# Kernel optimization log

Measured on AMD Instinct MI355X. Metric: run time of the kernel, lower is better.

Reference implementation:

```python
import jax, jax.numpy as jnp
import numpy as np

T = 100000


def setup_inputs() -> dict:
    key = jax.random.key(0)
    u = jax.random.normal(key, (1, T, 2), dtype=jnp.float32)
    M = jnp.array([20.0, 10.0], dtype=jnp.float32)
    C = jnp.array([10.0, 10.0, 10.0], dtype=jnp.float32)   # trainable damping
    K = jnp.array([2000.0, 1000.0, 5000.0], dtype=jnp.float32)
    x0 = jnp.zeros((1, 4), dtype=jnp.float32)              # [y1, v1, y2, v2]
    dt = jnp.asarray(0.002, dtype=jnp.float32)
    return {"u": u, "M": M, "C": C, "K": K, "x0": x0, "dt": dt}


def reference(u, M, C, K, x0, dt):
    # 2x2 coupled damping / stiffness matrices (same math as _fun)
    Cm = jnp.stack([jnp.stack([C[0] + C[1], -C[1]]),
                    jnp.stack([-C[1], C[2] + C[1]])])
    Km = jnp.stack([jnp.stack([K[0] + K[1], -K[1]]),
                    jnp.stack([-K[1], K[2] + K[1]])])

    def accel(z, v, ut):  # z, v, ut: [2]
        return (ut - Cm @ v - Km @ z) / M

    def step(carry, ut):
        y, v = carry
        k1 = accel(y, v, ut)
        y2 = y + v * (dt / 2.0); v2 = v + k1 * (dt / 2.0)
        k2 = accel(y2, v2, ut)
        y3 = y + v2 * (dt / 2.0); v3 = v + k2 * (dt / 2.0)
        k3 = accel(y3, v3, ut)
        y4 = y + v3 * dt; v4 = v + k3 * dt
        k4 = accel(y4, v4, ut)
        yn = y + (dt / 6.0) * (v + 2.0 * v2 + 2.0 * v3 + v4)
        vn = v + (dt / 6.0) * (k1 + 2.0 * k2 + 2.0 * k3 + k4)
        return (yn, vn), yn

    y0 = x0[0, ::2]   # positions [y1, y2]
    v0 = x0[0, 1::2]  # velocities [v1, v2]
    _, ys = jax.lax.scan(step, (y0, v0), u[0])  # ys: [T, 2]
    return ys[None]  # [1, T, 2] position sequence, matching RNN output y
```

## Files before the change

### kernel.cpp

```cpp
#include <hip/hip_runtime.h>


#define L_LOG2   6
#define L_CHUNK  64
#define SEG      8
#define NSEG     256
#define NCHUNK   (NSEG * SEG)
#define SMAX     16
#define NLEV     (SMAX - L_LOG2 + 1)

__device__ inline void accel_d(const double* M, const double* Cm, const double* Km,
                               const double* u, const double* z, const double* v, double* a) {
  a[0] = (u[0] - Cm[0] * v[0] - Cm[1] * v[1] - Km[0] * z[0] - Km[1] * z[1]) / M[0];
  a[1] = (u[1] - Cm[2] * v[0] - Cm[3] * v[1] - Km[2] * z[0] - Km[3] * z[1]) / M[1];
}

__device__ inline void rk4_step_d(const double* M, const double* Cm, const double* Km,
                                  double dt, double* y, double* v, const double* u) {
  double k1[2], k2[2], k3[2], k4[2];
  double y2[2], v2[2], y3[2], v3[2], y4[2], v4[2];
  double h = dt * 0.5;
  accel_d(M, Cm, Km, u, y, v, k1);
  y2[0] = y[0] + v[0] * h;  y2[1] = y[1] + v[1] * h;
  v2[0] = v[0] + k1[0] * h; v2[1] = v[1] + k1[1] * h;
  accel_d(M, Cm, Km, u, y2, v2, k2);
  y3[0] = y[0] + v2[0] * h;  y3[1] = y[1] + v2[1] * h;
  v3[0] = v[0] + k2[0] * h;  v3[1] = v[1] + k2[1] * h;
  accel_d(M, Cm, Km, u, y3, v3, k3);
  y4[0] = y[0] + v3[0] * dt; y4[1] = y[1] + v3[1] * dt;
  v4[0] = v[0] + k3[0] * dt; v4[1] = v[1] + k3[1] * dt;
  accel_d(M, Cm, Km, u, y4, v4, k4);
  double s = dt / 6.0;
  double yn0 = y[0] + s * (v[0] + 2.0 * v2[0] + 2.0 * v3[0] + v4[0]);
  double yn1 = y[1] + s * (v[1] + 2.0 * v2[1] + 2.0 * v3[1] + v4[1]);
  double vn0 = v[0] + s * (k1[0] + 2.0 * k2[0] + 2.0 * k3[0] + k4[0]);
  double vn1 = v[1] + s * (k1[1] + 2.0 * k2[1] + 2.0 * k3[1] + k4[1]);
  y[0] = yn0; y[1] = yn1; v[0] = vn0; v[1] = vn1;
}

__device__ inline void build_cols(const float* Mp, const float* Cp, const float* Kp,
                                  const float* dtp, float* Af, float* Bf, double* Ad) {
  int tid = threadIdx.x;
  if (tid < 6) {
    double M[2]  = {(double)Mp[0], (double)Mp[1]};
    double Cm[4] = {(double)Cp[0] + (double)Cp[1], -(double)Cp[1],
                    -(double)Cp[1], (double)Cp[2] + (double)Cp[1]};
    double Km[4] = {(double)Kp[0] + (double)Kp[1], -(double)Kp[1],
                    -(double)Kp[1], (double)Kp[2] + (double)Kp[1]};
    double dt = (double)dtp[0];
    double y[2] = {0, 0}, v[2] = {0, 0}, u[2] = {0, 0};
    if      (tid == 0) y[0] = 1.0;
    else if (tid == 1) y[1] = 1.0;
    else if (tid == 2) v[0] = 1.0;
    else if (tid == 3) v[1] = 1.0;
    else if (tid == 4) u[0] = 1.0;
    else               u[1] = 1.0;
    rk4_step_d(M, Cm, Km, dt, y, v, u);
    if (tid < 4) {
      if (Af) {
        Af[0 * 4 + tid] = (float)y[0]; Af[1 * 4 + tid] = (float)y[1];
        Af[2 * 4 + tid] = (float)v[0]; Af[3 * 4 + tid] = (float)v[1];
      }
      if (Ad) {
        Ad[0 * 4 + tid] = y[0]; Ad[1 * 4 + tid] = y[1];
        Ad[2 * 4 + tid] = v[0]; Ad[3 * 4 + tid] = v[1];
      }
    } else if (Bf) {
      int j = tid - 4;
      Bf[0 * 2 + j] = (float)y[0]; Bf[1 * 2 + j] = (float)y[1];
      Bf[2 * 2 + j] = (float)v[0]; Bf[3 * 2 + j] = (float)v[1];
    }
  }
}

__device__ inline float4 mv4(const float* A, float4 x) {
  float4 r;
  r.x = A[0]  * x.x + A[1]  * x.y + A[2]  * x.z + A[3]  * x.w;
  r.y = A[4]  * x.x + A[5]  * x.y + A[6]  * x.z + A[7]  * x.w;
  r.z = A[8]  * x.x + A[9]  * x.y + A[10] * x.z + A[11] * x.w;
  r.w = A[12] * x.x + A[13] * x.y + A[14] * x.z + A[15] * x.w;
  return r;
}
__device__ inline float4 f4add(float4 a, float4 b) {
  return make_float4(a.x + b.x, a.y + b.y, a.z + b.z, a.w + b.w);
}
__device__ inline float4 stepf(const float* a, const float* b, float4 s, float2 ut) {
  float4 r;
  r.x = a[0]  * s.x + a[1]  * s.y + a[2]  * s.z + a[3]  * s.w + b[0] * ut.x + b[1] * ut.y;
  r.y = a[4]  * s.x + a[5]  * s.y + a[6]  * s.z + a[7]  * s.w + b[2] * ut.x + b[3] * ut.y;
  r.z = a[8]  * s.x + a[9]  * s.y + a[10] * s.z + a[11] * s.w + b[4] * ut.x + b[5] * ut.y;
  r.w = a[12] * s.x + a[13] * s.y + a[14] * s.z + a[15] * s.w + b[6] * ut.x + b[7] * ut.y;
  return r;
}

__global__ __launch_bounds__(256) void kOffsets(
    const float* __restrict__ u, const float* M, const float* C, const float* K,
    const float* dtp, int T, float4* __restrict__ c_arr) {
  __shared__ float Af[16], Bf[8];
  build_cols(M, C, K, dtp, Af, Bf, nullptr);
  __syncthreads();
  float a[16], b[8];
#pragma unroll
  for (int e = 0; e < 16; ++e) a[e] = Af[e];
#pragma unroll
  for (int e = 0; e < 8; ++e) b[e] = Bf[e];

  int j  = blockIdx.x * blockDim.x + threadIdx.x;
  int t0 = j * L_CHUNK;
  const float2* u2 = (const float2*)u;
  float4 c = make_float4(0.f, 0.f, 0.f, 0.f);
  if (t0 + L_CHUNK <= T) {
#pragma unroll 4
    for (int i = 0; i < L_CHUNK; ++i) c = stepf(a, b, c, u2[t0 + i]);
  } else {
    for (int i = 0; i < L_CHUNK; ++i) {
      int t = t0 + i;
      if (t >= T) break;
      c = stepf(a, b, c, u2[t]);
    }
  }
  c_arr[j] = c;
}

__global__ __launch_bounds__(NSEG) void kScan(
    const float* M, const float* C, const float* K, const float* dtp,
    const float* x0, int T, const float4* __restrict__ c_arr, float4* __restrict__ s_arr) {
  __shared__ double Ad[16];
  __shared__ float  Gp[NLEV][16];
  __shared__ float4 S[NSEG];
  build_cols(M, C, K, dtp, nullptr, nullptr, Ad);
  __syncthreads();

  int tid = threadIdx.x;
  if (tid < 16) {
    double m = Ad[tid];
    int i = tid >> 2, j = tid & 3;
#pragma unroll
    for (int lvl = 1; lvl <= SMAX; ++lvl) {
      double acc = 0.0;
#pragma unroll
      for (int k = 0; k < 4; ++k)
        acc += __shfl(m, i * 4 + k) * __shfl(m, k * 4 + j);
      m = acc;
      if (lvl >= L_LOG2) Gp[lvl - L_LOG2][tid] = (float)m;
    }
  }
  __syncthreads();

  float G[16];
#pragma unroll
  for (int e = 0; e < 16; ++e) G[e] = Gp[0][e];

  float4 cj[SEG];
  int sbase = tid * SEG;
#pragma unroll
  for (int r = 0; r < SEG; ++r) cj[r] = c_arr[sbase + r];
  float4 o = cj[0];
#pragma unroll
  for (int r = 1; r < SEG; ++r) o = f4add(mv4(G, o), cj[r]);

  if (tid == 0) {
    float4 s0 = make_float4(x0[0], x0[2], x0[1], x0[3]);
    o = f4add(mv4(&Gp[3][0], s0), o);
  }
  S[tid] = o;
  __syncthreads();

#pragma unroll
  for (int k = 0; k < 8; ++k) {
    int off = 1 << k;
    float4 add = make_float4(0.f, 0.f, 0.f, 0.f);
    bool act = (tid >= off);
    if (act) add = mv4(&Gp[3 + k][0], S[tid - off]);
    __syncthreads();
    if (act) S[tid] = f4add(S[tid], add);
    __syncthreads();
  }

  float4 st;
  if (tid == 0) st = make_float4(x0[0], x0[2], x0[1], x0[3]);
  else          st = S[tid - 1];
#pragma unroll
  for (int r = 0; r < SEG; ++r) {
    s_arr[sbase + r] = st;
    st = f4add(mv4(G, st), cj[r]);
  }
}

__global__ __launch_bounds__(256) void kEmit(
    const float* __restrict__ u, const float* M, const float* C, const float* K,
    const float* dtp, int T, const float4* __restrict__ s_arr, float2* __restrict__ out) {
  __shared__ float Af[16], Bf[8];
  build_cols(M, C, K, dtp, Af, Bf, nullptr);
  __syncthreads();
  float a[16], b[8];
#pragma unroll
  for (int e = 0; e < 16; ++e) a[e] = Af[e];
#pragma unroll
  for (int e = 0; e < 8; ++e) b[e] = Bf[e];

  int j  = blockIdx.x * blockDim.x + threadIdx.x;
  int t0 = j * L_CHUNK;
  const float2* u2 = (const float2*)u;
  float4 s = s_arr[j];
  if (t0 + L_CHUNK <= T) {
#pragma unroll 4
    for (int i = 0; i < L_CHUNK; ++i) {
      int t = t0 + i;
      s = stepf(a, b, s, u2[t]);
      out[t] = make_float2(s.x, s.y);
    }
  } else {
    for (int i = 0; i < L_CHUNK; ++i) {
      int t = t0 + i;
      if (t >= T) break;
      s = stepf(a, b, s, u2[t]);
      out[t] = make_float2(s.x, s.y);
    }
  }
}

__global__ void kSerialAll(const float* u, const float* Mp, const float* Cp, const float* Kp,
                           const float* dtp, const float* x0, int T, float2* out) {
  if (threadIdx.x != 0 || blockIdx.x != 0) return;
  double M[2]  = {(double)Mp[0], (double)Mp[1]};
  double Cm[4] = {(double)Cp[0] + (double)Cp[1], -(double)Cp[1],
                  -(double)Cp[1], (double)Cp[2] + (double)Cp[1]};
  double Km[4] = {(double)Kp[0] + (double)Kp[1], -(double)Kp[1],
                  -(double)Kp[1], (double)Kp[2] + (double)Kp[1]};
  double dt = (double)dtp[0];
  double y[2] = {(double)x0[0], (double)x0[2]};
  double v[2] = {(double)x0[1], (double)x0[3]};
  for (int t = 0; t < T; ++t) {
    double uu[2] = {(double)u[2 * t], (double)u[2 * t + 1]};
    rk4_step_d(M, Cm, Km, dt, y, v, uu);
    out[t] = make_float2((float)y[0], (float)y[1]);
  }
}

extern "C" void kernel_launch(void* const* d_in, const int* in_sizes, int n_in,
                              void* d_out, int out_size, void* d_ws, size_t ws_size,
                              hipStream_t stream) {
  (void)n_in; (void)out_size;
  const float* u   = (const float*)d_in[0];
  const float* M   = (const float*)d_in[1];
  const float* C   = (const float*)d_in[2];
  const float* K   = (const float*)d_in[3];
  const float* x0  = (const float*)d_in[4];
  const float* dt  = (const float*)d_in[5];
  int T = in_sizes[0] / 2;
  float2* out = (float2*)d_out;

  size_t need = (size_t)2 * NCHUNK * sizeof(float4);
  if (ws_size < need || T > NCHUNK * L_CHUNK) {
    kSerialAll<<<1, 64, 0, stream>>>(u, M, C, K, dt, x0, T, out);
    return;
  }
  float4* c_arr = (float4*)d_ws;
  float4* s_arr = c_arr + NCHUNK;

  kOffsets<<<NCHUNK / 256, 256, 0, stream>>>(u, M, C, K, dt, T, c_arr);
  kScan<<<1, NSEG, 0, stream>>>(M, C, K, dt, x0, T, c_arr, s_arr);
  kEmit<<<NCHUNK / 256, 256, 0, stream>>>(u, M, C, K, dt, T, s_arr, out);
}
```

Measured before the change: 92.35 us.

## Shrink chunks to 16 steps, widen segment scan, vectorize u/out accesses

Chunk length drops from 64 to 16 steps and each scan thread now handles 25 chunks, so the offsets and emit kernels launch about four times as many threads (6400 chunks) and each serial chain is shorter. Because the segment span is no longer a power of two, the scan kernel now builds the needed matrix powers (A^16 and A^400 with its squarings) through explicit double-precision shuffle matmuls. Input and output accesses are vectorized to float4, two timesteps per load or store. The cost is a longer serial per-thread loop and more register pressure in the single-block scan kernel.

```diff
diff --git a/kernel.cpp b/kernel.cpp
--- a/kernel.cpp
+++ b/kernel.cpp
@@ -1,13 +1,10 @@
 #include <hip/hip_runtime.h>
 
 
-#define L_LOG2   6
-#define L_CHUNK  64
-#define SEG      8
+#define LSTEP    16
+#define SEG      25
 #define NSEG     256
-#define NCHUNK   (NSEG * SEG)
-#define SMAX     16
-#define NLEV     (SMAX - L_LOG2 + 1)
+#define NCHPAD   (NSEG * SEG)
 
 __device__ inline void accel_d(const double* M, const double* Cm, const double* Km,
                                const double* u, const double* z, const double* v, double* a) {
@@ -93,6 +90,14 @@
   return r;
 }
 
+__device__ inline double matmul16(double a, double b, int i, int j) {
+  double acc = 0.0;
+#pragma unroll
+  for (int k = 0; k < 4; ++k)
+    acc += __shfl(a, i * 4 + k) * __shfl(b, k * 4 + j);
+  return acc;
+}
+
 __global__ __launch_bounds__(256) void kOffsets(
     const float* __restrict__ u, const float* M, const float* C, const float* K,
     const float* dtp, int T, float4* __restrict__ c_arr) {
@@ -106,14 +111,19 @@
   for (int e = 0; e < 8; ++e) b[e] = Bf[e];
 
   int j  = blockIdx.x * blockDim.x + threadIdx.x;
-  int t0 = j * L_CHUNK;
-  const float2* u2 = (const float2*)u;
+  int t0 = j * LSTEP;
   float4 c = make_float4(0.f, 0.f, 0.f, 0.f);
-  if (t0 + L_CHUNK <= T) {
-#pragma unroll 4
-    for (int i = 0; i < L_CHUNK; ++i) c = stepf(a, b, c, u2[t0 + i]);
+  if (t0 + LSTEP <= T) {
+    const float4* u4 = (const float4*)(u + 2 * t0);
+#pragma unroll
+    for (int i = 0; i < LSTEP / 2; ++i) {
+      float4 uu = u4[i];
+      c = stepf(a, b, c, make_float2(uu.x, uu.y));
+      c = stepf(a, b, c, make_float2(uu.z, uu.w));
+    }
   } else {
-    for (int i = 0; i < L_CHUNK; ++i) {
+    const float2* u2 = (const float2*)u;
+    for (int i = 0; i < LSTEP; ++i) {
       int t = t0 + i;
       if (t >= T) break;
       c = stepf(a, b, c, u2[t]);
@@ -126,30 +136,34 @@
     const float* M, const float* C, const float* K, const float* dtp,
     const float* x0, int T, const float4* __restrict__ c_arr, float4* __restrict__ s_arr) {
   __shared__ double Ad[16];
-  __shared__ float  Gp[NLEV][16];
+  __shared__ float  Gs[16];
+  __shared__ float  Wp[8][16];
   __shared__ float4 S[NSEG];
   build_cols(M, C, K, dtp, nullptr, nullptr, Ad);
   __syncthreads();
 
   int tid = threadIdx.x;
   if (tid < 16) {
+    int i = tid >> 2, jj = tid & 3;
     double m = Ad[tid];
-    int i = tid >> 2, j = tid & 3;
-#pragma unroll
-    for (int lvl = 1; lvl <= SMAX; ++lvl) {
-      double acc = 0.0;
-#pragma unroll
-      for (int k = 0; k < 4; ++k)
-        acc += __shfl(m, i * 4 + k) * __shfl(m, k * 4 + j);
-      m = acc;
-      if (lvl >= L_LOG2) Gp[lvl - L_LOG2][tid] = (float)m;
-    }
+#pragma unroll
+    for (int l = 0; l < 4; ++l) m = matmul16(m, m, i, jj);
+    Gs[tid] = (float)m;
+    double t1 = m;
+    double t2  = matmul16(t1, t1, i, jj);
+    double t4  = matmul16(t2, t2, i, jj);
+    double t8  = matmul16(t4, t4, i, jj);
+    double t16 = matmul16(t8, t8, i, jj);
+    double w = matmul16(matmul16(t16, t8, i, jj), t1, i, jj);
+    Wp[0][tid] = (float)w;
+#pragma unroll
+    for (int k = 1; k < 8; ++k) { w = matmul16(w, w, i, jj); Wp[k][tid] = (float)w; }
   }
   __syncthreads();
 
   float G[16];
 #pragma unroll
-  for (int e = 0; e < 16; ++e) G[e] = Gp[0][e];
+  for (int e = 0; e < 16; ++e) G[e] = Gs[e];
 
   float4 cj[SEG];
   int sbase = tid * SEG;
@@ -159,10 +173,8 @@
 #pragma unroll
   for (int r = 1; r < SEG; ++r) o = f4add(mv4(G, o), cj[r]);
 
-  if (tid == 0) {
-    float4 s0 = make_float4(x0[0], x0[2], x0[1], x0[3]);
-    o = f4add(mv4(&Gp[3][0], s0), o);
-  }
+  float4 s0 = make_float4(x0[0], x0[2], x0[1], x0[3]);
+  if (tid == 0) o = f4add(mv4(&Wp[0][0], s0), o);
   S[tid] = o;
   __syncthreads();
 
@@ -171,15 +183,13 @@
     int off = 1 << k;
     float4 add = make_float4(0.f, 0.f, 0.f, 0.f);
     bool act = (tid >= off);
-    if (act) add = mv4(&Gp[3 + k][0], S[tid - off]);
+    if (act) add = mv4(&Wp[k][0], S[tid - off]);
     __syncthreads();
     if (act) S[tid] = f4add(S[tid], add);
     __syncthreads();
   }
 
-  float4 st;
-  if (tid == 0) st = make_float4(x0[0], x0[2], x0[1], x0[3]);
-  else          st = S[tid - 1];
+  float4 st = (tid == 0) ? s0 : S[tid - 1];
 #pragma unroll
   for (int r = 0; r < SEG; ++r) {
     s_arr[sbase + r] = st;
@@ -200,18 +210,22 @@
   for (int e = 0; e < 8; ++e) b[e] = Bf[e];
 
   int j  = blockIdx.x * blockDim.x + threadIdx.x;
-  int t0 = j * L_CHUNK;
-  const float2* u2 = (const float2*)u;
+  int t0 = j * LSTEP;
   float4 s = s_arr[j];
-  if (t0 + L_CHUNK <= T) {
-#pragma unroll 4
-    for (int i = 0; i < L_CHUNK; ++i) {
-      int t = t0 + i;
-      s = stepf(a, b, s, u2[t]);
-      out[t] = make_float2(s.x, s.y);
+  if (t0 + LSTEP <= T) {
+    const float4* u4 = (const float4*)(u + 2 * t0);
+    float4* o4 = (float4*)(out + t0);
+#pragma unroll
+    for (int i = 0; i < LSTEP / 2; ++i) {
+      float4 uu = u4[i];
+      s = stepf(a, b, s, make_float2(uu.x, uu.y));
+      float2 ya = make_float2(s.x, s.y);
+      s = stepf(a, b, s, make_float2(uu.z, uu.w));
+      o4[i] = make_float4(ya.x, ya.y, s.x, s.y);
     }
   } else {
-    for (int i = 0; i < L_CHUNK; ++i) {
+    const float2* u2 = (const float2*)u;
+    for (int i = 0; i < LSTEP; ++i) {
       int t = t0 + i;
       if (t >= T) break;
       s = stepf(a, b, s, u2[t]);
@@ -251,15 +265,15 @@
   int T = in_sizes[0] / 2;
   float2* out = (float2*)d_out;
 
-  size_t need = (size_t)2 * NCHUNK * sizeof(float4);
-  if (ws_size < need || T > NCHUNK * L_CHUNK) {
+  size_t need = (size_t)2 * NCHPAD * sizeof(float4);
+  if (ws_size < need || T > NCHPAD * LSTEP) {
     kSerialAll<<<1, 64, 0, stream>>>(u, M, C, K, dt, x0, T, out);
     return;
   }
   float4* c_arr = (float4*)d_ws;
-  float4* s_arr = c_arr + NCHUNK;
-
-  kOffsets<<<NCHUNK / 256, 256, 0, stream>>>(u, M, C, K, dt, T, c_arr);
+  float4* s_arr = c_arr + NCHPAD;
+
+  kOffsets<<<NCHPAD / 256, 256, 0, stream>>>(u, M, C, K, dt, T, c_arr);
   kScan<<<1, NSEG, 0, stream>>>(M, C, K, dt, x0, T, c_arr, s_arr);
-  kEmit<<<NCHUNK / 256, 256, 0, stream>>>(u, M, C, K, dt, T, s_arr, out);
-}
+  kEmit<<<NCHPAD / 256, 256, 0, stream>>>(u, M, C, K, dt, T, s_arr, out);
+}
```

Result: faster. 82.72 us (-10.4%).
